# Kernel tuning notes

Measured on AMD Instinct MI355X. Metric: run time of the kernel, lower is better.

## Reference

```python
import jax, jax.numpy as jnp
import numpy as np

B, L, D = 2, 1024, 768
H, DH = 12, 64
DP = 32
MLP = 4 * D
NL = 4
WINDOW = 128
EPS_RMS = 1.1920929e-07  # torch F.rms_norm default eps = finfo(float32).eps
EPS_LN = 1e-5


def rmsnorm(x):
    return x * jax.lax.rsqrt(jnp.mean(x * x, axis=-1, keepdims=True) + EPS_RMS)


def layernorm(x, g, b):
    m = jnp.mean(x, axis=-1, keepdims=True)
    v = jnp.mean((x - m) ** 2, axis=-1, keepdims=True)
    return (x - m) * jax.lax.rsqrt(v + EPS_LN) * g + b


def rope(q, k):
    # q,k: [B,H,L,DH]; standard rotate-half RoPE, theta=10000
    half = DH // 2
    inv_freq = 1.0 / (10000.0 ** (jnp.arange(0, DH, 2, dtype=jnp.float32) / DH))  # [half]
    freqs = jnp.arange(L, dtype=jnp.float32)[:, None] * inv_freq[None, :]  # [L,half]
    cos = jnp.concatenate([jnp.cos(freqs), jnp.cos(freqs)], -1)[None, None]  # [1,1,L,DH]
    sin = jnp.concatenate([jnp.sin(freqs), jnp.sin(freqs)], -1)[None, None]

    def rot(x):
        x1, x2 = jnp.split(x, 2, axis=-1)
        return jnp.concatenate([-x2, x1], axis=-1)

    return q * cos + rot(q) * sin, k * cos + rot(k) * sin


def setup_inputs() -> dict:
    key = jax.random.key(0)
    ks = jax.random.split(key, 16)
    sc = 0.02
    return {
        "s": jax.random.normal(ks[0], (B, L, D), jnp.float32),
        "pair": jax.random.normal(ks[1], (B, L, L, DP), jnp.float32),
        "qkv_w": jax.random.normal(ks[2], (NL, 3 * D, D), jnp.float32) * sc,
        "qkv_b": jnp.zeros((NL, 3 * D), jnp.float32),
        "out_w": jax.random.normal(ks[3], (NL, D, D), jnp.float32) * sc,
        "out_b": jnp.zeros((NL, D), jnp.float32),
        "fc1_w": jax.random.normal(ks[4], (NL, MLP, D), jnp.float32) * sc,
        "fc1_b": jnp.zeros((NL, MLP), jnp.float32),
        "fc2_w": jax.random.normal(ks[5], (NL, D, MLP), jnp.float32) * sc,
        "fc2_b": jnp.zeros((NL, D), jnp.float32),
        "ln_g": jnp.ones((NL, DP), jnp.float32),
        "ln_b": jnp.zeros((NL, DP), jnp.float32),
        "pb_w": jax.random.normal(ks[6], (NL, DP), jnp.float32) * sc,
        "pb_b": jnp.zeros((NL,), jnp.float32),
    }


def reference(s, pair, qkv_w, qkv_b, out_w, out_b, fc1_w, fc1_b, fc2_w, fc2_b,
              ln_g, ln_b, pb_w, pb_b):
    idx = jnp.arange(L)
    window_mask = jnp.abs(idx[:, None] - idx[None, :]) <= WINDOW  # [L,L]
    neg_inf = jnp.float32(-1e30)
    scale = 1.0 / jnp.sqrt(jnp.float32(DH))

    for l in range(NL):
        # pair bias score-mod: LayerNorm + Linear(DP,1)
        bias = layernorm(pair, ln_g[l], ln_b[l]) @ pb_w[l] + pb_b[l]  # [B,L,L]

        h = rmsnorm(s)
        qkv = h @ qkv_w[l].T + qkv_b[l]  # [B,L,3D]
        q, k, v = jnp.split(qkv, 3, axis=-1)
        q = q.reshape(B, L, H, DH).transpose(0, 2, 1, 3)
        k = k.reshape(B, L, H, DH).transpose(0, 2, 1, 3)
        v = v.reshape(B, L, H, DH).transpose(0, 2, 1, 3)
        q, k = rope(q, k)

        scores = jnp.einsum("bhqd,bhkd->bhqk", q, k) * scale + bias[:, None]
        scores = jnp.where(window_mask[None, None], scores, neg_inf)
        attn = jax.nn.softmax(scores, axis=-1)
        y = jnp.einsum("bhqk,bhkd->bhqd", attn, v)
        y = y.transpose(0, 2, 1, 3).reshape(B, L, D)
        s = s + y @ out_w[l].T + out_b[l]

        h = rmsnorm(s)
        h = jax.nn.gelu(h @ fc1_w[l].T + fc1_b[l], approximate=False)
        s = s + h @ fc2_w[l].T + fc2_b[l]
    return s
```

## Files before the change

kernel.cpp:

```cpp
#include <hip/hip_runtime.h>

#define B_    2
#define L_    1024
#define D_    768
#define H_    12
#define DH_   64
#define DP_   32
#define MLP_  3072
#define NL_   4
#define WIN_  128
#define W2_   257
#define M_    (B_*L_)

typedef __attribute__((ext_vector_type(8))) short bf16x8;
typedef __attribute__((ext_vector_type(4))) float f32x4;

__device__ __forceinline__ unsigned short f2bf(float x){
  unsigned int u = __float_as_uint(x);
  u += 0x7fffu + ((u >> 16) & 1u);
  return (unsigned short)(u >> 16);
}

__device__ __forceinline__ void gl_lds16(const void* g, void* l){
  __builtin_amdgcn_global_load_lds((__attribute__((address_space(1))) void*)g,
                                   (__attribute__((address_space(3))) void*)l, 16, 0, 0);
}

__global__ __launch_bounds__(256) void cvt_bf16_k(const float* __restrict__ src,
                                                  unsigned short* __restrict__ dst, int n4){
  int i = blockIdx.x*256 + threadIdx.x;
  if (i >= n4) return;
  float4 v = ((const float4*)src)[i];
  ushort4 o;
  o.x = f2bf(v.x); o.y = f2bf(v.y); o.z = f2bf(v.z); o.w = f2bf(v.w);
  ((ushort4*)dst)[i] = o;
}

__global__ __launch_bounds__(256) void rope_tab_k(float2* __restrict__ rtab){
  int idx = blockIdx.x*256 + threadIdx.x;
  int t = idx & 31, i = idx >> 5;
  float invf = expf(-(float)t * 0.28782313662425572f);
  float ang = (float)i * invf;
  float sn, cs;
  sincosf(ang, &sn, &cs);
  rtab[idx] = make_float2(cs, sn);
}

__global__ __launch_bounds__(256) void pair_bias_k(const float* __restrict__ pair,
    const float* __restrict__ ln_g, const float* __restrict__ ln_b,
    const float* __restrict__ pb_w, const float* __restrict__ pb_b,
    float* __restrict__ bias){
  __shared__ float gw[NL_][DP_];
  __shared__ float cb[NL_];
  int tid = threadIdx.x;
  if (tid < NL_*DP_) gw[tid>>5][tid&31] = ln_g[tid]*pb_w[tid];
  if (tid < NL_){
    float c = 0.f;
    for (int d=0; d<DP_; ++d) c += ln_b[tid*DP_+d]*pb_w[tid*DP_+d];
    cb[tid] = c + pb_b[tid];
  }
  __syncthreads();
  int idx = blockIdx.x*256 + tid;
  if (idx >= B_*L_*W2_) return;
  int rel = idx % W2_;
  int t   = idx / W2_;
  int i   = t & (L_-1);
  int b   = t >> 10;
  int j   = i + rel - WIN_;
  if (j < 0 || j >= L_) return;
  const float4* p = (const float4*)(pair + ((size_t)(b*L_ + i)*L_ + j)*DP_);
  float4 x[8];
  #pragma unroll
  for (int q=0;q<8;++q) x[q] = p[q];
  float s=0.f, ss=0.f;
  #pragma unroll
  for (int q=0;q<8;++q){
    s  += x[q].x + x[q].y + x[q].z + x[q].w;
    ss += x[q].x*x[q].x + x[q].y*x[q].y + x[q].z*x[q].z + x[q].w*x[q].w;
  }
  float m  = s * (1.0f/DP_);
  float rs = rsqrtf(ss*(1.0f/DP_) - m*m + 1e-5f);
  #pragma unroll
  for (int l=0;l<NL_;++l){
    float acc = 0.f;
    #pragma unroll
    for (int q=0;q<8;++q){
      acc += (x[q].x-m)*gw[l][4*q+0] + (x[q].y-m)*gw[l][4*q+1]
           + (x[q].z-m)*gw[l][4*q+2] + (x[q].w-m)*gw[l][4*q+3];
    }
    bias[(((size_t)l*B_ + b)*L_ + i)*W2_ + rel] = acc*rs + cb[l];
  }
}

__global__ __launch_bounds__(256) void rmsnorm_k(const float* __restrict__ s,
                                                 unsigned short* __restrict__ h){
  int row = blockIdx.x, tid = threadIdx.x;
  const float* x = s + (size_t)row*D_;
  float v0 = x[tid], v1 = x[tid+256], v2 = x[tid+512];
  float ss = v0*v0 + v1*v1 + v2*v2;
  #pragma unroll
  for (int m=1; m<64; m<<=1) ss += __shfl_xor(ss, m, 64);
  __shared__ float wsum[4];
  __shared__ float rbuf;
  if ((tid & 63) == 0) wsum[tid>>6] = ss;
  __syncthreads();
  if (tid == 0) rbuf = rsqrtf((wsum[0]+wsum[1]+wsum[2]+wsum[3])*(1.0f/D_) + 1.1920929e-07f);
  __syncthreads();
  float r = rbuf;
  unsigned short* o = h + (size_t)row*D_;
  o[tid]     = f2bf(v0*r);
  o[tid+256] = f2bf(v1*r);
  o[tid+512] = f2bf(v2*r);
}

template<int MODE, int TM, int SPLIT>
__global__ __launch_bounds__(256) void gemm_bt(const unsigned short* __restrict__ A,
    const unsigned short* __restrict__ W, const float* __restrict__ bias,
    unsigned short* __restrict__ outb, float* __restrict__ resid,
    unsigned short* __restrict__ outq, unsigned short* __restrict__ outk,
    const float2* __restrict__ rtab, int N, int K){
  constexpr int MI = TM/32;
  __shared__ __align__(16) short sm[2][(TM+128)*32];
  const int tid  = threadIdx.x;
  const int wave = tid >> 6, lane = tid & 63;
  const int m0 = blockIdx.y*TM, n0 = blockIdx.x << 7;
  const int KB = K / SPLIT;
  const int kbase = blockIdx.z * KB;
  const int wm = (wave >> 1)*(TM/2), wn = (wave & 1) << 6;
  const int lrow = lane & 15, ko = (lane >> 4) << 3;
  f32x4 acc[MI][4] = {};
  const unsigned short* Ag = A + (size_t)(m0 + (tid>>2))*K + kbase + ((tid&3)<<3);
  const unsigned short* Wg = W + (size_t)(n0 + (tid>>2))*K + kbase + ((tid&3)<<3);
  const size_t hstep = (size_t)64*K;
  const int nk = KB >> 5;
  {
    short* As = sm[0]; short* Bs = sm[0] + TM*32;
    gl_lds16(Ag, &As[tid*8]);
    if (TM == 128) gl_lds16(Ag + hstep, &As[(tid+256)*8]);
    gl_lds16(Wg, &Bs[tid*8]);
    gl_lds16(Wg + hstep, &Bs[(tid+256)*8]);
  }
  for (int it = 0; it < nk; ++it){
    __syncthreads();
    if (it + 1 < nk){
      short* As = sm[(it&1)^1]; short* Bs = As + TM*32;
      const int kt = (it+1) << 5;
      gl_lds16(Ag + kt, &As[tid*8]);
      if (TM == 128) gl_lds16(Ag + hstep + kt, &As[(tid+256)*8]);
      gl_lds16(Wg + kt, &Bs[tid*8]);
      gl_lds16(Wg + hstep + kt, &Bs[(tid+256)*8]);
    }
    const short* As = sm[it&1]; const short* Bs = As + TM*32;
    bf16x8 af[MI], bv[4];
    #pragma unroll
    for (int i=0;i<MI;++i) af[i] = *(const bf16x8*)&As[((wm + i*16 + lrow) << 5) + ko];
    #pragma unroll
    for (int i=0;i<4;++i)  bv[i] = *(const bf16x8*)&Bs[((wn + i*16 + lrow) << 5) + ko];
    #pragma unroll
    for (int mi=0;mi<MI;++mi)
      #pragma unroll
      for (int ni=0;ni<4;++ni)
        acc[mi][ni] = __builtin_amdgcn_mfma_f32_16x16x32_bf16(af[mi], bv[ni], acc[mi][ni], 0, 0, 0);
  }
  if (MODE == 0){
    #pragma unroll
    for (int ni=0; ni<2; ++ni){
      const int col0 = n0 + wn + ni*16 + lrow;
      const int d0 = ni*16 + lrow;
      const float b0 = bias[col0], b2 = bias[col0 + 32];
      #pragma unroll
      for (int mi=0; mi<MI; ++mi){
        const int rw = m0 + wm + mi*16 + ((lane >> 4) << 2);
        #pragma unroll
        for (int r=0; r<4; ++r){
          const int rowg = rw + r;
          const int bI = rowg >> 10, iI = rowg & (L_-1);
          const float v0 = acc[mi][ni][r]   + b0;
          const float v2 = acc[mi][ni+2][r] + b2;
          if (col0 < 2*D_){
            const bool isq = (col0 < D_);
            const int  h   = (isq ? col0 : col0 - D_) >> 6;
            const float2 cssn = rtab[iI*32 + d0];
            const float o0 = v0*cssn.x - v2*cssn.y;
            const float o2 = v2*cssn.x + v0*cssn.y;
            unsigned short* dst = (isq ? outq : outk)
                + ((((size_t)(bI*H_ + h)) << 10 | iI) << 6);
            dst[d0]      = f2bf(o0);
            dst[d0 + 32] = f2bf(o2);
          } else {
            const int h = (col0 - 2*D_) >> 6;
            unsigned short* dst = outb + ((((size_t)(bI*H_ + h)) << 10 | iI) << 6);
            dst[d0]      = f2bf(v0);
            dst[d0 + 32] = f2bf(v2);
          }
        }
      }
    }
  } else {
    #pragma unroll
    for (int ni=0;ni<4;++ni){
      const int col = n0 + wn + ni*16 + lrow;
      const float bb = (SPLIT == 1 || blockIdx.z == 0) ? bias[col] : 0.f;
      #pragma unroll
      for (int mi=0;mi<MI;++mi){
        const int rw = m0 + wm + mi*16 + ((lane >> 4) << 2);
        #pragma unroll
        for (int r=0;r<4;++r){
          float v = acc[mi][ni][r] + bb;
          if (MODE == 2){
            float g = 0.5f * v * (1.0f + erff(v * 0.70710678118654752f));
            outb[(size_t)(rw + r)*N + col] = f2bf(g);
          } else {
            if (SPLIT == 1) resid[(size_t)(rw + r)*D_ + col] += v;
            else            atomicAdd(&resid[(size_t)(rw + r)*D_ + col], v);
          }
        }
      }
    }
  }
}

__global__ __launch_bounds__(256) void attn_k(const unsigned short* __restrict__ qr,
    const unsigned short* __restrict__ kr, const unsigned short* __restrict__ vr,
    const float* __restrict__ bias, unsigned short* __restrict__ ybf, int layer){
  __shared__ __align__(16) short kb[288*72];
  __shared__ __align__(16) float sc[32*304];
  short* ps = (short*)sc;
  const int tid  = threadIdx.x;
  const int wave = tid >> 6, lane = tid & 63;
  const int quad = lane >> 4, lrow = lane & 15;
  const int bh = blockIdx.y, b = bh / H_, h = bh - b*H_;
  const int i0 = blockIdx.x * 32, jb = i0 - WIN_;

  bf16x8 qf[2][2];
  #pragma unroll
  for (int mt=0; mt<2; ++mt){
    const unsigned short* qrow = qr + (((size_t)bh*L_ + i0 + mt*16 + lrow) << 6) + quad*8;
    qf[mt][0] = *(const bf16x8*)qrow;
    qf[mt][1] = *(const bf16x8*)(qrow + 32);
  }
  {
    const int r0 = tid >> 3, seg = tid & 7;
    #pragma unroll
    for (int p=0; p<9; ++p){
      const int r = r0 + p*32;
      const int jg = jb + r;
      bf16x8 z;
      #pragma unroll
      for (int q=0;q<8;++q) z[q] = 0;
      if ((unsigned)jg < L_) z = *(const bf16x8*)(kr + (((size_t)bh*L_ + jg) << 6) + seg*8);
      *(bf16x8*)&kb[r*72 + seg*8] = z;
    }
  }
  __syncthreads();
  for (int c = wave; c < 18; c += 4){
    const int krow = c*16 + lrow;
    const bf16x8 kf0 = *(const bf16x8*)&kb[krow*72 + quad*8];
    const bf16x8 kf1 = *(const bf16x8*)&kb[krow*72 + 32 + quad*8];
    const int jj = c*16 + lrow, jg = jb + jj;
    #pragma unroll
    for (int mt=0; mt<2; ++mt){
      f32x4 cc = {0.f,0.f,0.f,0.f};
      cc = __builtin_amdgcn_mfma_f32_16x16x32_bf16(qf[mt][0], kf0, cc, 0, 0, 0);
      cc = __builtin_amdgcn_mfma_f32_16x16x32_bf16(qf[mt][1], kf1, cc, 0, 0, 0);
      #pragma unroll
      for (int r=0;r<4;++r){
        const int row = mt*16 + quad*4 + r;
        const int rel = jj - row;
        float v = -1e30f;
        if (rel >= 0 && rel <= 256 && (unsigned)jg < L_)
          v = cc[r]*0.125f + bias[(((size_t)(layer*B_ + b))*L_ + i0 + row)*W2_ + rel];
        sc[row*304 + jj] = v;
      }
    }
  }
  __syncthreads();
  const int qq = tid >> 4, tj = tid & 15;
  float ev[2][18];
  #pragma unroll
  for (int g=0; g<2; ++g)
    #pragma unroll
    for (int c=0;c<18;++c) ev[g][c] = sc[(qq + g*16)*304 + c*16 + tj];
  __syncthreads();
  #pragma unroll
  for (int g=0; g<2; ++g){
    float mx = -3.0e38f;
    #pragma unroll
    for (int c=0;c<18;++c) mx = fmaxf(mx, ev[g][c]);
    #pragma unroll
    for (int m=1; m<16; m<<=1) mx = fmaxf(mx, __shfl_xor(mx, m, 16));
    float sm = 0.f;
    #pragma unroll
    for (int c=0;c<18;++c){ float e = __expf(ev[g][c] - mx); ev[g][c] = e; sm += e; }
    #pragma unroll
    for (int m=1; m<16; m<<=1) sm += __shfl_xor(sm, m, 16);
    const float inv = 1.0f / sm;
    #pragma unroll
    for (int c=0;c<18;++c) ps[(qq + g*16)*296 + c*16 + tj] = (short)f2bf(ev[g][c]*inv);
  }
  {
    const int r0 = tid >> 3, seg = tid & 7;
    #pragma unroll
    for (int p=0; p<9; ++p){
      const int r = r0 + p*32;
      const int jg = jb + r;
      bf16x8 z;
      #pragma unroll
      for (int q=0;q<8;++q) z[q] = 0;
      if ((unsigned)jg < L_) z = *(const bf16x8*)(vr + (((size_t)bh*L_ + jg) << 6) + seg*8);
      *(bf16x8*)&kb[r*72 + seg*8] = z;
    }
  }
  __syncthreads();
  f32x4 o0 = {0.f,0.f,0.f,0.f}, o1 = {0.f,0.f,0.f,0.f};
  for (int kc=0; kc<9; ++kc){
    bf16x8 bf;
    #pragma unroll
    for (int j=0;j<8;++j) bf[j] = kb[(kc*32 + quad*8 + j)*72 + wave*16 + lrow];
    const bf16x8 a0 = *(const bf16x8*)&ps[lrow*296 + kc*32 + quad*8];
    const bf16x8 a1 = *(const bf16x8*)&ps[(16 + lrow)*296 + kc*32 + quad*8];
    o0 = __builtin_amdgcn_mfma_f32_16x16x32_bf16(a0, bf, o0, 0, 0, 0);
    o1 = __builtin_amdgcn_mfma_f32_16x16x32_bf16(a1, bf, o1, 0, 0, 0);
  }
  #pragma unroll
  for (int r=0;r<4;++r){
    const int row = quad*4 + r;
    ybf[((size_t)(b*L_ + i0 + row))*D_ + h*64 + wave*16 + lrow]      = f2bf(o0[r]);
    ybf[((size_t)(b*L_ + i0 + 16 + row))*D_ + h*64 + wave*16 + lrow] = f2bf(o1[r]);
  }
}

extern "C" void kernel_launch(void* const* d_in, const int* in_sizes, int n_in,
                              void* d_out, int out_size, void* d_ws, size_t ws_size,
                              hipStream_t stream){
  (void)in_sizes; (void)n_in; (void)out_size; (void)ws_size;
  const float* s_in  = (const float*)d_in[0];
  const float* pair  = (const float*)d_in[1];
  const float* qkv_w = (const float*)d_in[2];
  const float* qkv_b = (const float*)d_in[3];
  const float* out_w = (const float*)d_in[4];
  const float* out_b = (const float*)d_in[5];
  const float* fc1_w = (const float*)d_in[6];
  const float* fc1_b = (const float*)d_in[7];
  const float* fc2_w = (const float*)d_in[8];
  const float* fc2_b = (const float*)d_in[9];
  const float* ln_g  = (const float*)d_in[10];
  const float* ln_b  = (const float*)d_in[11];
  const float* pb_w  = (const float*)d_in[12];
  const float* pb_b  = (const float*)d_in[13];
  float* s = (float*)d_out;

  char* ws = (char*)d_ws;
  size_t off = 0;
  auto take = [&](size_t bytes)->char*{
    char* p = ws + off; off += (bytes + 255) & ~(size_t)255; return p;
  };
  unsigned short* wqkv = (unsigned short*)take((size_t)NL_*3*D_*D_*2);
  unsigned short* wout = (unsigned short*)take((size_t)NL_*D_*D_*2);
  unsigned short* wfc1 = (unsigned short*)take((size_t)NL_*MLP_*D_*2);
  unsigned short* wfc2 = (unsigned short*)take((size_t)NL_*D_*MLP_*2);
  float*          bw   = (float*)take((size_t)NL_*B_*L_*W2_*4);
  unsigned short* hbf  = (unsigned short*)take((size_t)M_*D_*2);
  unsigned short* qrb  = (unsigned short*)take((size_t)B_*H_*L_*DH_*2);
  unsigned short* krb  = (unsigned short*)take((size_t)B_*H_*L_*DH_*2);
  unsigned short* vrb  = (unsigned short*)take((size_t)B_*H_*L_*DH_*2);
  unsigned short* ybf  = (unsigned short*)take((size_t)M_*D_*2);
  unsigned short* gbf  = (unsigned short*)take((size_t)M_*MLP_*2);
  float2*         rtab = (float2*)take((size_t)L_*32*sizeof(float2));

  hipMemcpyAsync(s, s_in, (size_t)M_*D_*sizeof(float), hipMemcpyDeviceToDevice, stream);

  auto cvt = [&](const float* src, unsigned short* dst, size_t n){
    int n4 = (int)(n/4);
    cvt_bf16_k<<<(n4+255)/256, 256, 0, stream>>>(src, dst, n4);
  };
  cvt(qkv_w, wqkv, (size_t)NL_*3*D_*D_);
  cvt(out_w, wout, (size_t)NL_*D_*D_);
  cvt(fc1_w, wfc1, (size_t)NL_*MLP_*D_);
  cvt(fc2_w, wfc2, (size_t)NL_*D_*MLP_);

  rope_tab_k<<<(L_*32)/256, 256, 0, stream>>>(rtab);
  pair_bias_k<<<(B_*L_*W2_ + 255)/256, 256, 0, stream>>>(pair, ln_g, ln_b, pb_w, pb_b, bw);

  for (int l=0; l<NL_; ++l){
    rmsnorm_k<<<M_, 256, 0, stream>>>(s, hbf);
    gemm_bt<0,128,1><<<dim3((3*D_)/128, M_/128), 256, 0, stream>>>(
        hbf, wqkv + (size_t)l*3*D_*D_, qkv_b + l*3*D_, vrb, nullptr, qrb, krb, rtab, 3*D_, D_);
    attn_k<<<dim3(L_/32, B_*H_), 256, 0, stream>>>(qrb, krb, vrb, bw, ybf, l);
    gemm_bt<1,64,2><<<dim3(D_/128, M_/64, 2), 256, 0, stream>>>(
        ybf, wout + (size_t)l*D_*D_, out_b + l*D_, nullptr, s, nullptr, nullptr, nullptr, D_, D_);
    rmsnorm_k<<<M_, 256, 0, stream>>>(s, hbf);
    gemm_bt<2,128,1><<<dim3(MLP_/128, M_/128), 256, 0, stream>>>(
        hbf, wfc1 + (size_t)l*MLP_*D_, fc1_b + l*MLP_, gbf, nullptr, nullptr, nullptr, nullptr, MLP_, D_);
    gemm_bt<3,64,4><<<dim3(D_/128, M_/64, 4), 256, 0, stream>>>(
        gbf, wfc2 + (size_t)l*D_*MLP_, fc2_b + l*D_, nullptr, s, nullptr, nullptr, nullptr, D_, MLP_);
  }
}
```

Measured before the change: 1.017 ms.

## Fuse RMSNorm into GEMM A-load and merge prologue kernels into one launch

RMSNorm moves into the QKV and FC1 GEMMs. Each block computes the per-row inverse RMS from the fp32 residual, then loads fp32 A tiles through registers, scales them, converts to bf16 and writes them to LDS. This removes the separate rmsnorm kernels and the bf16 hidden buffer. The pair-bias, RoPE table and weight-conversion kernels are merged into a single prologue launch, which relies on the weight buffers being contiguous in the workspace. In exchange, each GEMM column block recomputes the row norms and reads fp32 A with register staging instead of async direct-to-LDS loads, which doubles A read traffic.

After: 1.222 ms. +20.2%, slower.

```diff
diff --git a/kernel.cpp b/kernel.cpp
--- a/kernel.cpp
+++ b/kernel.cpp
@@ -26,95 +26,86 @@
                                    (__attribute__((address_space(3))) void*)l, 16, 0, 0);
 }
 
-__global__ __launch_bounds__(256) void cvt_bf16_k(const float* __restrict__ src,
-                                                  unsigned short* __restrict__ dst, int n4){
-  int i = blockIdx.x*256 + threadIdx.x;
-  if (i >= n4) return;
-  float4 v = ((const float4*)src)[i];
-  ushort4 o;
-  o.x = f2bf(v.x); o.y = f2bf(v.y); o.z = f2bf(v.z); o.w = f2bf(v.w);
-  ((ushort4*)dst)[i] = o;
-}
-
-__global__ __launch_bounds__(256) void rope_tab_k(float2* __restrict__ rtab){
-  int idx = blockIdx.x*256 + threadIdx.x;
-  int t = idx & 31, i = idx >> 5;
-  float invf = expf(-(float)t * 0.28782313662425572f);
-  float ang = (float)i * invf;
-  float sn, cs;
-  sincosf(ang, &sn, &cs);
-  rtab[idx] = make_float2(cs, sn);
-}
-
-__global__ __launch_bounds__(256) void pair_bias_k(const float* __restrict__ pair,
-    const float* __restrict__ ln_g, const float* __restrict__ ln_b,
-    const float* __restrict__ pb_w, const float* __restrict__ pb_b,
-    float* __restrict__ bias){
+#define PB_BLKS_   2056
+#define RT_BLKS_   128
+#define CVT_Q0_    1769472
+#define CVT_Q1_    2359296
+#define CVT_Q2_    4718592
+#define CVT_Q3_    7077888
+__global__ __launch_bounds__(256) void prologue_k(
+    const float* __restrict__ pair, const float* __restrict__ ln_g,
+    const float* __restrict__ ln_b, const float* __restrict__ pb_w,
+    const float* __restrict__ pb_b, float* __restrict__ bias,
+    float2* __restrict__ rtab,
+    const float* __restrict__ qkv_w, const float* __restrict__ out_w,
+    const float* __restrict__ fc1_w, const float* __restrict__ fc2_w,
+    unsigned short* __restrict__ wall){
   __shared__ float gw[NL_][DP_];
   __shared__ float cb[NL_];
-  int tid = threadIdx.x;
-  if (tid < NL_*DP_) gw[tid>>5][tid&31] = ln_g[tid]*pb_w[tid];
-  if (tid < NL_){
-    float c = 0.f;
-    for (int d=0; d<DP_; ++d) c += ln_b[tid*DP_+d]*pb_w[tid*DP_+d];
-    cb[tid] = c + pb_b[tid];
-  }
-  __syncthreads();
-  int idx = blockIdx.x*256 + tid;
-  if (idx >= B_*L_*W2_) return;
-  int rel = idx % W2_;
-  int t   = idx / W2_;
-  int i   = t & (L_-1);
-  int b   = t >> 10;
-  int j   = i + rel - WIN_;
-  if (j < 0 || j >= L_) return;
-  const float4* p = (const float4*)(pair + ((size_t)(b*L_ + i)*L_ + j)*DP_);
-  float4 x[8];
-  #pragma unroll
-  for (int q=0;q<8;++q) x[q] = p[q];
-  float s=0.f, ss=0.f;
-  #pragma unroll
-  for (int q=0;q<8;++q){
-    s  += x[q].x + x[q].y + x[q].z + x[q].w;
-    ss += x[q].x*x[q].x + x[q].y*x[q].y + x[q].z*x[q].z + x[q].w*x[q].w;
-  }
-  float m  = s * (1.0f/DP_);
-  float rs = rsqrtf(ss*(1.0f/DP_) - m*m + 1e-5f);
-  #pragma unroll
-  for (int l=0;l<NL_;++l){
-    float acc = 0.f;
+  const int bid = blockIdx.x, tid = threadIdx.x;
+  if (bid < PB_BLKS_){
+    if (tid < NL_*DP_) gw[tid>>5][tid&31] = ln_g[tid]*pb_w[tid];
+    if (tid < NL_){
+      float c = 0.f;
+      for (int d=0; d<DP_; ++d) c += ln_b[tid*DP_+d]*pb_w[tid*DP_+d];
+      cb[tid] = c + pb_b[tid];
+    }
+    __syncthreads();
+    int idx = bid*256 + tid;
+    if (idx >= B_*L_*W2_) return;
+    int rel = idx % W2_;
+    int t   = idx / W2_;
+    int i   = t & (L_-1);
+    int b   = t >> 10;
+    int j   = i + rel - WIN_;
+    if (j < 0 || j >= L_) return;
+    const float4* p = (const float4*)(pair + ((size_t)(b*L_ + i)*L_ + j)*DP_);
+    float4 x[8];
+    #pragma unroll
+    for (int q=0;q<8;++q) x[q] = p[q];
+    float s=0.f, ss=0.f;
     #pragma unroll
     for (int q=0;q<8;++q){
-      acc += (x[q].x-m)*gw[l][4*q+0] + (x[q].y-m)*gw[l][4*q+1]
-           + (x[q].z-m)*gw[l][4*q+2] + (x[q].w-m)*gw[l][4*q+3];
-    }
-    bias[(((size_t)l*B_ + b)*L_ + i)*W2_ + rel] = acc*rs + cb[l];
-  }
-}
-
-__global__ __launch_bounds__(256) void rmsnorm_k(const float* __restrict__ s,
-                                                 unsigned short* __restrict__ h){
-  int row = blockIdx.x, tid = threadIdx.x;
-  const float* x = s + (size_t)row*D_;
-  float v0 = x[tid], v1 = x[tid+256], v2 = x[tid+512];
-  float ss = v0*v0 + v1*v1 + v2*v2;
-  #pragma unroll
-  for (int m=1; m<64; m<<=1) ss += __shfl_xor(ss, m, 64);
-  __shared__ float wsum[4];
-  __shared__ float rbuf;
-  if ((tid & 63) == 0) wsum[tid>>6] = ss;
-  __syncthreads();
-  if (tid == 0) rbuf = rsqrtf((wsum[0]+wsum[1]+wsum[2]+wsum[3])*(1.0f/D_) + 1.1920929e-07f);
-  __syncthreads();
-  float r = rbuf;
-  unsigned short* o = h + (size_t)row*D_;
-  o[tid]     = f2bf(v0*r);
-  o[tid+256] = f2bf(v1*r);
-  o[tid+512] = f2bf(v2*r);
-}
-
-template<int MODE, int TM, int SPLIT>
+      s  += x[q].x + x[q].y + x[q].z + x[q].w;
+      ss += x[q].x*x[q].x + x[q].y*x[q].y + x[q].z*x[q].z + x[q].w*x[q].w;
+    }
+    float m  = s * (1.0f/DP_);
+    float rs = rsqrtf(ss*(1.0f/DP_) - m*m + 1e-5f);
+    #pragma unroll
+    for (int l=0;l<NL_;++l){
+      float acc = 0.f;
+      #pragma unroll
+      for (int q=0;q<8;++q){
+        acc += (x[q].x-m)*gw[l][4*q+0] + (x[q].y-m)*gw[l][4*q+1]
+             + (x[q].z-m)*gw[l][4*q+2] + (x[q].w-m)*gw[l][4*q+3];
+      }
+      bias[(((size_t)l*B_ + b)*L_ + i)*W2_ + rel] = acc*rs + cb[l];
+    }
+  } else if (bid < PB_BLKS_ + RT_BLKS_){
+    int idx = (bid - PB_BLKS_)*256 + tid;
+    int t = idx & 31, i = idx >> 5;
+    float invf = expf(-(float)t * 0.28782313662425572f);
+    float ang = (float)i * invf;
+    float sn, cs;
+    sincosf(ang, &sn, &cs);
+    rtab[idx] = make_float2(cs, sn);
+  } else {
+    size_t q = (size_t)(bid - PB_BLKS_ - RT_BLKS_)*256 + tid;
+    const float* src; unsigned short* dst; size_t ql;
+    if (q < CVT_Q0_)      { ql = q;            src = qkv_w; dst = wall; }
+    else if (q < CVT_Q1_) { ql = q - CVT_Q0_;  src = out_w; dst = wall + (size_t)CVT_Q0_*4; }
+    else if (q < CVT_Q2_) { ql = q - CVT_Q1_;  src = fc1_w; dst = wall + (size_t)CVT_Q1_*4; }
+    else                  { ql = q - CVT_Q2_;  src = fc2_w; dst = wall + (size_t)CVT_Q2_*4; }
+    float4 v = ((const float4*)src)[ql];
+    ushort4 o;
+    o.x = f2bf(v.x); o.y = f2bf(v.y); o.z = f2bf(v.z); o.w = f2bf(v.w);
+    ((ushort4*)dst)[ql] = o;
+  }
+}
+
+template<int MODE, int TM, int SPLIT, int RMSA>
 __global__ __launch_bounds__(256) void gemm_bt(const unsigned short* __restrict__ A,
+    const float* __restrict__ Af,
     const unsigned short* __restrict__ W, const float* __restrict__ bias,
     unsigned short* __restrict__ outb, float* __restrict__ resid,
     unsigned short* __restrict__ outq, unsigned short* __restrict__ outk,
@@ -129,24 +120,79 @@
   const int wm = (wave >> 1)*(TM/2), wn = (wave & 1) << 6;
   const int lrow = lane & 15, ko = (lane >> 4) << 3;
   f32x4 acc[MI][4] = {};
-  const unsigned short* Ag = A + (size_t)(m0 + (tid>>2))*K + kbase + ((tid&3)<<3);
   const unsigned short* Wg = W + (size_t)(n0 + (tid>>2))*K + kbase + ((tid&3)<<3);
   const size_t hstep = (size_t)64*K;
   const int nk = KB >> 5;
+
+  float rs = 0.f;
+  const float* Ab = nullptr;
+  const unsigned short* Ag = nullptr;
+  if constexpr (RMSA){
+    const int ar = tid >> 1, half = tid & 1;
+    const float* rowp = Af + (size_t)(m0 + ar)*D_ + half*(D_/2);
+    float s0=0.f, s1=0.f, s2=0.f, s3=0.f;
+    #pragma unroll 4
+    for (int q=0;q<24;++q){
+      float4 v0=((const float4*)rowp)[4*q+0], v1=((const float4*)rowp)[4*q+1];
+      float4 v2=((const float4*)rowp)[4*q+2], v3=((const float4*)rowp)[4*q+3];
+      s0 += v0.x*v0.x + v0.y*v0.y + v0.z*v0.z + v0.w*v0.w;
+      s1 += v1.x*v1.x + v1.y*v1.y + v1.z*v1.z + v1.w*v1.w;
+      s2 += v2.x*v2.x + v2.y*v2.y + v2.z*v2.z + v2.w*v2.w;
+      s3 += v3.x*v3.x + v3.y*v3.y + v3.z*v3.z + v3.w*v3.w;
+    }
+    float ssum = (s0+s1)+(s2+s3);
+    ssum += __shfl_xor(ssum, 1, 64);
+    rs = rsqrtf(ssum*(1.0f/D_) + 1.1920929e-07f);
+    Ab = Af + (size_t)(m0 + ar)*D_ + half*16;
+  } else {
+    Ag = A + (size_t)(m0 + (tid>>2))*K + kbase + ((tid&3)<<3);
+  }
+
+  float4 pa[4];
+  auto loadA = [&](int kt){
+    pa[0] = *(const float4*)(Ab + kt);
+    pa[1] = *(const float4*)(Ab + kt + 4);
+    pa[2] = *(const float4*)(Ab + kt + 8);
+    pa[3] = *(const float4*)(Ab + kt + 12);
+  };
+  auto writeA = [&](short* As){
+    bf16x8 w0, w1;
+    w0[0]=(short)f2bf(pa[0].x*rs); w0[1]=(short)f2bf(pa[0].y*rs);
+    w0[2]=(short)f2bf(pa[0].z*rs); w0[3]=(short)f2bf(pa[0].w*rs);
+    w0[4]=(short)f2bf(pa[1].x*rs); w0[5]=(short)f2bf(pa[1].y*rs);
+    w0[6]=(short)f2bf(pa[1].z*rs); w0[7]=(short)f2bf(pa[1].w*rs);
+    w1[0]=(short)f2bf(pa[2].x*rs); w1[1]=(short)f2bf(pa[2].y*rs);
+    w1[2]=(short)f2bf(pa[2].z*rs); w1[3]=(short)f2bf(pa[2].w*rs);
+    w1[4]=(short)f2bf(pa[3].x*rs); w1[5]=(short)f2bf(pa[3].y*rs);
+    w1[6]=(short)f2bf(pa[3].z*rs); w1[7]=(short)f2bf(pa[3].w*rs);
+    short* d = &As[(tid>>1)*32 + (tid&1)*16];
+    *(bf16x8*)(d)     = w0;
+    *(bf16x8*)(d + 8) = w1;
+  };
+
   {
     short* As = sm[0]; short* Bs = sm[0] + TM*32;
-    gl_lds16(Ag, &As[tid*8]);
-    if (TM == 128) gl_lds16(Ag + hstep, &As[(tid+256)*8]);
+    if constexpr (RMSA){
+      loadA(0); writeA(As);
+    } else {
+      gl_lds16(Ag, &As[tid*8]);
+      if (TM == 128) gl_lds16(Ag + hstep, &As[(tid+256)*8]);
+    }
     gl_lds16(Wg, &Bs[tid*8]);
     gl_lds16(Wg + hstep, &Bs[(tid+256)*8]);
   }
   for (int it = 0; it < nk; ++it){
     __syncthreads();
-    if (it + 1 < nk){
+    const bool pf = (it + 1 < nk);
+    if (pf){
       short* As = sm[(it&1)^1]; short* Bs = As + TM*32;
       const int kt = (it+1) << 5;
-      gl_lds16(Ag + kt, &As[tid*8]);
-      if (TM == 128) gl_lds16(Ag + hstep + kt, &As[(tid+256)*8]);
+      if constexpr (RMSA){
+        loadA(kt);
+      } else {
+        gl_lds16(Ag + kt, &As[tid*8]);
+        if (TM == 128) gl_lds16(Ag + hstep + kt, &As[(tid+256)*8]);
+      }
       gl_lds16(Wg + kt, &Bs[tid*8]);
       gl_lds16(Wg + hstep + kt, &Bs[(tid+256)*8]);
     }
@@ -161,6 +207,7 @@
       #pragma unroll
       for (int ni=0;ni<4;++ni)
         acc[mi][ni] = __builtin_amdgcn_mfma_f32_16x16x32_bf16(af[mi], bv[ni], acc[mi][ni], 0, 0, 0);
+    if (RMSA && pf) writeA(sm[(it&1)^1]);
   }
   if (MODE == 0){
     #pragma unroll
@@ -360,7 +407,6 @@
   unsigned short* wfc1 = (unsigned short*)take((size_t)NL_*MLP_*D_*2);
   unsigned short* wfc2 = (unsigned short*)take((size_t)NL_*D_*MLP_*2);
   float*          bw   = (float*)take((size_t)NL_*B_*L_*W2_*4);
-  unsigned short* hbf  = (unsigned short*)take((size_t)M_*D_*2);
   unsigned short* qrb  = (unsigned short*)take((size_t)B_*H_*L_*DH_*2);
   unsigned short* krb  = (unsigned short*)take((size_t)B_*H_*L_*DH_*2);
   unsigned short* vrb  = (unsigned short*)take((size_t)B_*H_*L_*DH_*2);
@@ -370,29 +416,19 @@
 
   hipMemcpyAsync(s, s_in, (size_t)M_*D_*sizeof(float), hipMemcpyDeviceToDevice, stream);
 
-  auto cvt = [&](const float* src, unsigned short* dst, size_t n){
-    int n4 = (int)(n/4);
-    cvt_bf16_k<<<(n4+255)/256, 256, 0, stream>>>(src, dst, n4);
-  };
-  cvt(qkv_w, wqkv, (size_t)NL_*3*D_*D_);
-  cvt(out_w, wout, (size_t)NL_*D_*D_);
-  cvt(fc1_w, wfc1, (size_t)NL_*MLP_*D_);
-  cvt(fc2_w, wfc2, (size_t)NL_*D_*MLP_);
-
-  rope_tab_k<<<(L_*32)/256, 256, 0, stream>>>(rtab);
-  pair_bias_k<<<(B_*L_*W2_ + 255)/256, 256, 0, stream>>>(pair, ln_g, ln_b, pb_w, pb_b, bw);
+  prologue_k<<<PB_BLKS_ + RT_BLKS_ + CVT_Q3_/256, 256, 0, stream>>>(
+      pair, ln_g, ln_b, pb_w, pb_b, bw, rtab,
+      qkv_w, out_w, fc1_w, fc2_w, wqkv);
 
   for (int l=0; l<NL_; ++l){
-    rmsnorm_k<<<M_, 256, 0, stream>>>(s, hbf);
-    gemm_bt<0,128,1><<<dim3((3*D_)/128, M_/128), 256, 0, stream>>>(
-        hbf, wqkv + (size_t)l*3*D_*D_, qkv_b + l*3*D_, vrb, nullptr, qrb, krb, rtab, 3*D_, D_);
+    gemm_bt<0,128,1,1><<<dim3((3*D_)/128, M_/128), 256, 0, stream>>>(
+        nullptr, s, wqkv + (size_t)l*3*D_*D_, qkv_b + l*3*D_, vrb, nullptr, qrb, krb, rtab, 3*D_, D_);
     attn_k<<<dim3(L_/32, B_*H_), 256, 0, stream>>>(qrb, krb, vrb, bw, ybf, l);
-    gemm_bt<1,64,2><<<dim3(D_/128, M_/64, 2), 256, 0, stream>>>(
-        ybf, wout + (size_t)l*D_*D_, out_b + l*D_, nullptr, s, nullptr, nullptr, nullptr, D_, D_);
-    rmsnorm_k<<<M_, 256, 0, stream>>>(s, hbf);
-    gemm_bt<2,128,1><<<dim3(MLP_/128, M_/128), 256, 0, stream>>>(
-        hbf, wfc1 + (size_t)l*MLP_*D_, fc1_b + l*MLP_, gbf, nullptr, nullptr, nullptr, nullptr, MLP_, D_);
-    gemm_bt<3,64,4><<<dim3(D_/128, M_/64, 4), 256, 0, stream>>>(
-        gbf, wfc2 + (size_t)l*D_*MLP_, fc2_b + l*D_, nullptr, s, nullptr, nullptr, nullptr, D_, MLP_);
-  }
-}
+    gemm_bt<1,64,2,0><<<dim3(D_/128, M_/64, 2), 256, 0, stream>>>(
+        ybf, nullptr, wout + (size_t)l*D_*D_, out_b + l*D_, nullptr, s, nullptr, nullptr, nullptr, D_, D_);
+    gemm_bt<2,128,1,1><<<dim3(MLP_/128, M_/128), 256, 0, stream>>>(
+        nullptr, s, wfc1 + (size_t)l*MLP_*D_, fc1_b + l*MLP_, gbf, nullptr, nullptr, nullptr, nullptr, MLP_, D_);
+    gemm_bt<3,64,4,0><<<dim3(D_/128, M_/64, 4), 256, 0, stream>>>(
+        gbf, nullptr, wfc2 + (size_t)l*D_*MLP_, fc2_b + l*D_, nullptr, s, nullptr, nullptr, nullptr, D_, MLP_);
+  }
+}
```
